# Performance work log

Hardware: AMD Instinct MI355X
Metric: run time of the kernel (lower is better)

Reference implementation:

```python
import jax, jax.numpy as jnp
import numpy as np

B, C, H_IMG, W_IMG = 16, 384, 56, 56
NUM_HEADS = 6
HEAD_DIM = C // NUM_HEADS
BN_EPS = 1e-5


def _bn(x, gamma, beta, mean, var):
    # x: [b, ch, n] or [b, ch, h, w]; per-channel affine normalization (eval-mode BatchNorm)
    shape = (1, -1) + (1,) * (x.ndim - 2)
    scale = (gamma / jnp.sqrt(var + BN_EPS)).reshape(shape)
    shift = (beta - mean * gamma / jnp.sqrt(var + BN_EPS)).reshape(shape)
    return x * scale + shift


def setup_inputs() -> dict:
    key = jax.random.key(0)
    ks = jax.random.split(key, 12)
    c2 = 2 * C
    return {
        "x": jax.random.normal(ks[0], (B, C, H_IMG, W_IMG), jnp.float32),
        "qk_w": jax.random.normal(ks[1], (c2, C // 2), jnp.float32) * 0.05,
        "qk_gamma": jax.random.uniform(ks[2], (c2,), jnp.float32, 0.5, 1.5),
        "qk_beta": jax.random.normal(ks[3], (c2,), jnp.float32) * 0.1,
        "qk_mean": jax.random.normal(ks[4], (c2,), jnp.float32) * 0.1,
        "qk_var": jax.random.uniform(ks[5], (c2,), jnp.float32, 0.5, 1.5),
        "pe_w": jax.random.normal(ks[6], (C, 1, 3, 3), jnp.float32) * 0.1,
        "pe_gamma": jax.random.uniform(ks[7], (C,), jnp.float32, 0.5, 1.5),
        "pe_beta": jax.random.normal(ks[8], (C,), jnp.float32) * 0.1,
        "pe_mean": jax.random.normal(ks[9], (C,), jnp.float32) * 0.1,
        "pe_var": jax.random.uniform(ks[10], (C,), jnp.float32, 0.5, 1.5),
    }


def reference(x, qk_w, qk_gamma, qk_beta, qk_mean, qk_var,
              pe_w, pe_gamma, pe_beta, pe_mean, pe_var):
    b, c, h, w = x.shape
    n = h * w
    s = n ** (-0.5)
    nh, hd = NUM_HEADS, HEAD_DIM

    # grouped (groups=2) 1x1 conv: out channels [0:c] from input [0:c/2], [c:2c] from [c/2:c]
    xg = x.reshape(b, 2, c // 2, n)                       # [b, 2, c/2, n]
    wg = qk_w.reshape(2, c, c // 2)                       # [group, out_per_group, in_per_group]
    qk = jnp.einsum('bgin,goi->bgon', xg, wg).reshape(b, 2 * c, n)
    qk = _bn(qk, qk_gamma, qk_beta, qk_mean, qk_var)
    qk = jax.nn.elu(qk) + 1.0

    qk = qk.reshape(b, 2, nh, hd, n)
    q, k = qk[:, 0], qk[:, 1]                             # [b, H, d, n]
    v = x.reshape(b, nh, hd, n)                           # [b, H, d, n]

    # kv = (k*s) @ (v^T * s): [b, H, d, d]
    kv = jnp.einsum('bhdn,bhen->bhde', k * s, v * s)
    # numerator: q^T @ kv -> [b, H, n, d]
    num = jnp.einsum('bhdn,bhde->bhne', q, kv)
    # denominator: q^T @ mean_n(k) -> [b, H, n]
    den = jnp.einsum('bhdn,bhd->bhn', q, k.mean(axis=-1)) + 1e-6
    attn = (num / den[..., None]).transpose(0, 1, 3, 2).reshape(b, c, h, w)

    # depthwise 3x3 conv positional encoding on v (= x) + BN
    pe = jax.lax.conv_general_dilated(
        x, pe_w, window_strides=(1, 1), padding=((1, 1), (1, 1)),
        feature_group_count=c, dimension_numbers=('NCHW', 'OIHW', 'NCHW'))
    pe = _bn(pe, pe_gamma, pe_beta, pe_mean, pe_var)

    return attn + pe
```

## Files before the change

### kernel.cpp

```cpp
#include <hip/hip_runtime.h>
#include <math.h>

#define N_SP 3136
#define BN_EPS 1e-5f

typedef __attribute__((ext_vector_type(8))) short short8;
typedef __attribute__((ext_vector_type(4))) float f32x4;

#define QK_SZ   (16*2*384*N_SP)
#define KVP_OFF (QK_SZ)
#define KVP_SZ  (16*6*7*64*80)
#define KVT_OFF (KVP_OFF + KVP_SZ)
#define KVT_FSZ (2*96*80*64/2)
#define WH_OFF  (KVT_OFF + KVT_FSZ)
#define WSPLIT_N (2*384*192)

__device__ __forceinline__ void bsplit(float f, ushort& h, ushort& l) {
    uint u = __float_as_uint(f);
    uint hr = (u + 0x7FFFu + ((u >> 16) & 1u)) >> 16;
    h = (ushort)hr;
    float fh = __uint_as_float(hr << 16);
    float fl = f - fh;
    uint v = __float_as_uint(fl);
    l = (ushort)((v + 0x7FFFu + ((v >> 16) & 1u)) >> 16);
}

__global__ __launch_bounds__(256) void p0_wsplit(
    const float* __restrict__ qk_w, ushort* __restrict__ wh, ushort* __restrict__ wl)
{
    int idx = blockIdx.x * 256 + threadIdx.x;
    if (idx >= WSPLIT_N) return;
    ushort h, l;
    bsplit(qk_w[idx], h, l);
    wh[idx] = h;
    wl[idx] = l;
}

__global__ __launch_bounds__(256) void k1_qk_mfma(
    const float* __restrict__ x, const ushort* __restrict__ wh, const ushort* __restrict__ wl,
    const float* __restrict__ gamma, const float* __restrict__ beta,
    const float* __restrict__ mean, const float* __restrict__ var,
    float* __restrict__ qk_out)
{
    __shared__ __align__(16) ushort Ah[8192];
    __shared__ __align__(16) ushort Al[8192];
    __shared__ __align__(16) ushort Bh[4096];
    __shared__ __align__(16) ushort Bl[4096];

    const int bx = blockIdx.x;
    const int by = blockIdx.y;
    const int bz = blockIdx.z;
    const int b = bz >> 1, gg = bz & 1;
    const int t = threadIdx.x;
    const int lane = t & 63, wv = t >> 6;
    const int wr = wv >> 1, wc = wv & 1;
    const int lg = lane >> 4, l15 = lane & 15;

    f32x4 acc[4][2];
    #pragma unroll
    for (int m = 0; m < 4; ++m)
        #pragma unroll
        for (int nf = 0; nf < 2; ++nf)
            acc[m][nf] = (f32x4){0.f, 0.f, 0.f, 0.f};

    const float* xg = x + (size_t)(b * 384 + gg * 192) * N_SP + bx * 64;
    const ushort* whg = wh + (gg * 384 + by * 128) * 192;
    const ushort* wlg = wl + (gg * 384 + by * 128) * 192;

    for (int kt = 0; kt < 3; ++kt) {
        #pragma unroll
        for (int li = 0; li < 4; ++li) {
            int c = li * 256 + t;
            int row = c >> 3, kb = c & 7;
            int goff = row * 192 + kt * 64 + kb * 8;
            float4 vh = *(const float4*)(whg + goff);
            float4 vl = *(const float4*)(wlg + goff);
            int ch = (row * 8 + (kb ^ (row & 7))) * 8;
            *(float4*)&Ah[ch] = vh;
            *(float4*)&Al[ch] = vl;
        }
        #pragma unroll
        for (int li = 0; li < 2; ++li) {
            int idx = li * 256 + t;
            int kp = idx >> 4;
            int nq = idx & 15;
            int k0 = kp * 2;
            const float* px = xg + (size_t)(kt * 64 + k0) * N_SP + nq * 4;
            float4 v0 = *(const float4*)px;
            float4 v1 = *(const float4*)(px + N_SP);
            ushort h0[4], l0[4], h1[4], l1[4];
            float a0[4] = {v0.x, v0.y, v0.z, v0.w};
            float a1[4] = {v1.x, v1.y, v1.z, v1.w};
            #pragma unroll
            for (int i = 0; i < 4; ++i) { bsplit(a0[i], h0[i], l0[i]); bsplit(a1[i], h1[i], l1[i]); }
            int kb = k0 >> 3, ks = (k0 & 6) >> 1;
            #pragma unroll
            for (int i = 0; i < 4; ++i) {
                int n = nq * 4 + i;
                int chunk = n * 8 + (kb ^ ((n >> 1) & 7));
                ((uint*)Bh)[chunk * 4 + ks] = (uint)h0[i] | ((uint)h1[i] << 16);
                ((uint*)Bl)[chunk * 4 + ks] = (uint)l0[i] | ((uint)l1[i] << 16);
            }
        }
        __syncthreads();
        #pragma unroll
        for (int s = 0; s < 2; ++s) {
            short8 ah[4], al[4], bh[2], bl[2];
            int kb = s * 4 + lg;
            #pragma unroll
            for (int m = 0; m < 4; ++m) {
                int row = wr * 64 + m * 16 + l15;
                int ch = (row * 8 + (kb ^ (row & 7))) * 8;
                ah[m] = *(const short8*)&Ah[ch];
                al[m] = *(const short8*)&Al[ch];
            }
            #pragma unroll
            for (int nf = 0; nf < 2; ++nf) {
                int n = wc * 32 + nf * 16 + l15;
                int ch = (n * 8 + (kb ^ ((n >> 1) & 7))) * 8;
                bh[nf] = *(const short8*)&Bh[ch];
                bl[nf] = *(const short8*)&Bl[ch];
            }
            #pragma unroll
            for (int m = 0; m < 4; ++m)
                #pragma unroll
                for (int nf = 0; nf < 2; ++nf) {
                    acc[m][nf] = __builtin_amdgcn_mfma_f32_16x16x32_bf16(ah[m], bh[nf], acc[m][nf], 0, 0, 0);
                    acc[m][nf] = __builtin_amdgcn_mfma_f32_16x16x32_bf16(ah[m], bl[nf], acc[m][nf], 0, 0, 0);
                    acc[m][nf] = __builtin_amdgcn_mfma_f32_16x16x32_bf16(al[m], bh[nf], acc[m][nf], 0, 0, 0);
                }
        }
        __syncthreads();
    }

    float* scs = (float*)Bh;
    float* shs = scs + 128;
    if (t < 128) {
        int ch = gg * 384 + by * 128 + t;
        float sc = gamma[ch] / sqrtf(var[ch] + BN_EPS);
        scs[t] = sc;
        shs[t] = beta[ch] - mean[ch] * sc;
    }
    __syncthreads();

    size_t obase = ((size_t)(b * 2 + gg) * 384 + by * 128) * N_SP + bx * 64 + wc * 32;
    #pragma unroll
    for (int m = 0; m < 4; ++m)
        #pragma unroll
        for (int nf = 0; nf < 2; ++nf) {
            #pragma unroll
            for (int r = 0; r < 4; ++r) {
                int orow = wr * 64 + m * 16 + lg * 4 + r;
                float v = acc[m][nf][r] * scs[orow] + shs[orow];
                v = v > 0.f ? v + 1.f : __expf(v);
                qk_out[obase + (size_t)orow * N_SP + nf * 16 + l15] = v;
            }
        }
}

__global__ __launch_bounds__(256) void k2_kv_mfma(
    const float* __restrict__ x, const float* __restrict__ qk,
    float* __restrict__ kv_part)
{
    __shared__ __align__(16) ushort Kh[4096], Kl[4096];
    __shared__ __align__(16) ushort Vh[5120], Vl[5120];

    const int chunk = blockIdx.x;
    const int h = blockIdx.y, b = blockIdx.z;
    const int t = threadIdx.x;
    const int lane = t & 63, wv = t >> 6;
    const int lg = lane >> 4, l15 = lane & 15;

    const float* kp = qk + (size_t)((b*2+1)*384 + h*64) * N_SP;
    const float* vp = x  + (size_t)(b*384 + h*64) * N_SP;

    #pragma unroll
    for (int li = 0; li < 4; ++li) {
        int idx = li * 256 + t;
        int row = 64 + (idx >> 6), col = idx & 63;
        int off = (row * 8 + ((col >> 3) ^ (row & 7))) * 8 + (col & 7);
        Vh[off] = (row == 64) ? (ushort)0x3F80 : (ushort)0;
        Vl[off] = 0;
    }

    f32x4 acc[5];
    #pragma unroll
    for (int nf = 0; nf < 5; ++nf) acc[nf] = (f32x4){0.f, 0.f, 0.f, 0.f};

    for (int sub = 0; sub < 7; ++sub) {
        int n0 = chunk * 448 + sub * 64;
        #pragma unroll
        for (int li = 0; li < 4; ++li) {
            int idx = li * 256 + t;
            int row = idx >> 4, sc = idx & 15;
            int off = (row * 8 + ((sc >> 1) ^ (row & 7))) * 8 + (sc & 1) * 4;
            float4 kf = *(const float4*)&kp[(size_t)row * N_SP + n0 + sc * 4];
            ushort h0,h1,h2,h3,l0,l1,l2,l3;
            bsplit(kf.x,h0,l0); bsplit(kf.y,h1,l1); bsplit(kf.z,h2,l2); bsplit(kf.w,h3,l3);
            ((uint*)&Kh[off])[0] = (uint)h0 | ((uint)h1 << 16);
            ((uint*)&Kh[off])[1] = (uint)h2 | ((uint)h3 << 16);
            ((uint*)&Kl[off])[0] = (uint)l0 | ((uint)l1 << 16);
            ((uint*)&Kl[off])[1] = (uint)l2 | ((uint)l3 << 16);
            float4 vf = *(const float4*)&vp[(size_t)row * N_SP + n0 + sc * 4];
            bsplit(vf.x,h0,l0); bsplit(vf.y,h1,l1); bsplit(vf.z,h2,l2); bsplit(vf.w,h3,l3);
            ((uint*)&Vh[off])[0] = (uint)h0 | ((uint)h1 << 16);
            ((uint*)&Vh[off])[1] = (uint)h2 | ((uint)h3 << 16);
            ((uint*)&Vl[off])[0] = (uint)l0 | ((uint)l1 << 16);
            ((uint*)&Vl[off])[1] = (uint)l2 | ((uint)l3 << 16);
        }
        __syncthreads();
        #pragma unroll
        for (int s = 0; s < 2; ++s) {
            int arow = wv * 16 + l15;
            int akb = (s * 4 + lg) ^ (arow & 7);
            short8 ah = *(const short8*)&Kh[(arow * 8 + akb) * 8];
            short8 al = *(const short8*)&Kl[(arow * 8 + akb) * 8];
            #pragma unroll
            for (int nf = 0; nf < 5; ++nf) {
                int brow = nf * 16 + l15;
                int bkb = (s * 4 + lg) ^ (brow & 7);
                short8 bh = *(const short8*)&Vh[(brow * 8 + bkb) * 8];
                short8 bl = *(const short8*)&Vl[(brow * 8 + bkb) * 8];
                acc[nf] = __builtin_amdgcn_mfma_f32_16x16x32_bf16(ah, bh, acc[nf], 0, 0, 0);
                acc[nf] = __builtin_amdgcn_mfma_f32_16x16x32_bf16(ah, bl, acc[nf], 0, 0, 0);
                acc[nf] = __builtin_amdgcn_mfma_f32_16x16x32_bf16(al, bh, acc[nf], 0, 0, 0);
            }
        }
        __syncthreads();
    }

    size_t base = (size_t)((b*6 + h)*7 + chunk) * 64 * 80;
    #pragma unroll
    for (int nf = 0; nf < 5; ++nf)
        #pragma unroll
        for (int r = 0; r < 4; ++r) {
            int d = wv * 16 + lg * 4 + r;
            kv_part[base + (size_t)d * 80 + nf * 16 + l15] = acc[nf][r];
        }
}

__global__ __launch_bounds__(256) void k2b_reduce(
    const float* __restrict__ kv_part,
    ushort* __restrict__ kvt_h, ushort* __restrict__ kvt_l)
{
    const int bh = blockIdx.x;
    const int t = threadIdx.x;
    const float inv_n = 1.0f / (float)N_SP;
    const float* base = kv_part + (size_t)bh * 7 * 64 * 80;
    ushort* oh = kvt_h + (size_t)bh * 80 * 64;
    ushort* ol = kvt_l + (size_t)bh * 80 * 64;
    for (int i = t; i < 80 * 64; i += 256) {
        int e = i >> 6, d = i & 63;
        float s = 0.f;
        if (e <= 64) {
            #pragma unroll
            for (int c = 0; c < 7; ++c) s += base[(size_t)(c * 64 + d) * 80 + e];
            s *= inv_n;
        }
        ushort h, l;
        bsplit(s, h, l);
        oh[i] = h; ol[i] = l;
    }
}

#define ATT_STRIDE 68
__global__ __launch_bounds__(256) void k3_attn_pe(
    const float* __restrict__ x, const float* __restrict__ qk,
    const ushort* __restrict__ kvt_h, const ushort* __restrict__ kvt_l,
    const float* __restrict__ pw,
    const float* __restrict__ pgamma, const float* __restrict__ pbeta,
    const float* __restrict__ pmean, const float* __restrict__ pvar,
    float* __restrict__ out)
{
    __shared__ __align__(16) float SBF[ATT_STRIDE * 64 + 64];
    ushort* Qh = (ushort*)SBF;
    ushort* Ql = Qh + 4096;

    const int bx = blockIdx.x;
    const int h = blockIdx.y, b = blockIdx.z;
    const int t = threadIdx.x;
    const int lane = t & 63, wv = t >> 6;
    const int lg = lane >> 4, l15 = lane & 15;
    const int n0 = bx * 64;
    const float* qp = qk + (size_t)((b*2+0)*384 + h*64) * N_SP + n0;

    #pragma unroll
    for (int li = 0; li < 2; ++li) {
        int idx = li * 256 + t;
        int kp2 = idx >> 4;
        int nq = idx & 15;
        int k0 = kp2 * 2;
        const float* px = qp + (size_t)k0 * N_SP + nq * 4;
        float4 v0 = *(const float4*)px;
        float4 v1 = *(const float4*)(px + N_SP);
        ushort h0[4], l0[4], h1[4], l1[4];
        float a0[4] = {v0.x, v0.y, v0.z, v0.w};
        float a1[4] = {v1.x, v1.y, v1.z, v1.w};
        #pragma unroll
        for (int i = 0; i < 4; ++i) { bsplit(a0[i], h0[i], l0[i]); bsplit(a1[i], h1[i], l1[i]); }
        int kb = k0 >> 3, ks = (k0 & 6) >> 1;
        #pragma unroll
        for (int i = 0; i < 4; ++i) {
            int n = nq * 4 + i;
            int chunk = n * 8 + (kb ^ ((n >> 1) & 7));
            ((uint*)Qh)[chunk * 4 + ks] = (uint)h0[i] | ((uint)h1[i] << 16);
            ((uint*)Ql)[chunk * 4 + ks] = (uint)l0[i] | ((uint)l1[i] << 16);
        }
    }
    __syncthreads();

    short8 bqh[2], bql[2];
    #pragma unroll
    for (int s = 0; s < 2; ++s) {
        int n = wv * 16 + l15;
        int chunk = n * 8 + ((s * 4 + lg) ^ ((n >> 1) & 7));
        bqh[s] = *(const short8*)&Qh[chunk * 8];
        bql[s] = *(const short8*)&Ql[chunk * 8];
    }
    __syncthreads();

    const ushort* ahb = kvt_h + (size_t)(b*6 + h) * 80 * 64;
    const ushort* alb = kvt_l + (size_t)(b*6 + h) * 80 * 64;
    f32x4 acc[5];
    #pragma unroll
    for (int m = 0; m < 5; ++m) acc[m] = (f32x4){0.f, 0.f, 0.f, 0.f};
    #pragma unroll
    for (int s = 0; s < 2; ++s) {
        #pragma unroll
        for (int m = 0; m < 5; ++m) {
            int off = (m * 16 + l15) * 64 + (s * 4 + lg) * 8;
            short8 ah = *(const short8*)&ahb[off];
            short8 al = *(const short8*)&alb[off];
            acc[m] = __builtin_amdgcn_mfma_f32_16x16x32_bf16(ah, bqh[s], acc[m], 0, 0, 0);
            acc[m] = __builtin_amdgcn_mfma_f32_16x16x32_bf16(ah, bql[s], acc[m], 0, 0, 0);
            acc[m] = __builtin_amdgcn_mfma_f32_16x16x32_bf16(al, bqh[s], acc[m], 0, 0, 0);
        }
    }

    {
        int ncol = wv * 16 + l15;
        #pragma unroll
        for (int m = 0; m < 4; ++m)
            #pragma unroll
            for (int r = 0; r < 4; ++r)
                SBF[(m * 16 + lg * 4 + r) * ATT_STRIDE + ncol] = acc[m][r];
        if (lg == 0)
            SBF[ATT_STRIDE * 64 + ncol] = acc[4][0];
    }
    __syncthreads();

    const int tx = t & 15, ty = t >> 4;
    const int p0 = n0 + tx * 4;
    const int y = p0 / 56, xc = p0 % 56;
    float den[4];
    #pragma unroll
    for (int p = 0; p < 4; ++p) den[p] = SBF[ATT_STRIDE * 64 + tx * 4 + p] + 1e-6f;
    #pragma unroll
    for (int j = 0; j < 4; ++j) {
        int cc = ty * 4 + j;
        int c = h * 64 + cc;
        const float* xp = x + ((size_t)b * 384 + c) * N_SP;
        float s6[3][6];
        #pragma unroll
        for (int dy = 0; dy < 3; ++dy) {
            int yy = y + dy - 1;
            bool yok = (yy >= 0) && (yy < 56);
            float4 mid = make_float4(0.f, 0.f, 0.f, 0.f);
            float lf = 0.f, rt = 0.f;
            if (yok) {
                const float* xr = xp + yy * 56;
                mid = *(const float4*)&xr[xc];
                if (xc > 0)  lf = xr[xc - 1];
                if (xc < 52) rt = xr[xc + 4];
            }
            s6[dy][0] = lf;  s6[dy][1] = mid.x; s6[dy][2] = mid.y;
            s6[dy][3] = mid.z; s6[dy][4] = mid.w; s6[dy][5] = rt;
        }
        float w9[9];
        #pragma unroll
        for (int q = 0; q < 9; ++q) w9[q] = pw[c * 9 + q];
        float sc2 = pgamma[c] / sqrtf(pvar[c] + BN_EPS);
        float sh2 = pbeta[c] - pmean[c] * sc2;
        float4 r;
        float* pr = (float*)&r;
        #pragma unroll
        for (int p = 0; p < 4; ++p) {
            float conv = 0.f;
            #pragma unroll
            for (int dy = 0; dy < 3; ++dy)
                #pragma unroll
                for (int dx = 0; dx < 3; ++dx)
                    conv += w9[dy * 3 + dx] * s6[dy][p + dx];
            float num = SBF[cc * ATT_STRIDE + tx * 4 + p];
            pr[p] = num / den[p] + (conv * sc2 + sh2);
        }
        *(float4*)&out[((size_t)b * 384 + c) * N_SP + p0] = r;
    }
}

extern "C" void kernel_launch(void* const* d_in, const int* in_sizes, int n_in,
                              void* d_out, int out_size, void* d_ws, size_t ws_size,
                              hipStream_t stream)
{
    const float* x        = (const float*)d_in[0];
    const float* qk_w     = (const float*)d_in[1];
    const float* qk_gamma = (const float*)d_in[2];
    const float* qk_beta  = (const float*)d_in[3];
    const float* qk_mean  = (const float*)d_in[4];
    const float* qk_var   = (const float*)d_in[5];
    const float* pe_w     = (const float*)d_in[6];
    const float* pe_gamma = (const float*)d_in[7];
    const float* pe_beta  = (const float*)d_in[8];
    const float* pe_mean  = (const float*)d_in[9];
    const float* pe_var   = (const float*)d_in[10];
    float* out = (float*)d_out;

    float* ws      = (float*)d_ws;
    float* qk      = ws;
    float* kv_part = ws + KVP_OFF;
    ushort* kvt_h  = (ushort*)(ws + KVT_OFF);
    ushort* kvt_l  = kvt_h + 96 * 80 * 64;
    ushort* whp    = (ushort*)(ws + WH_OFF);
    ushort* wlp    = whp + WSPLIT_N;

    hipLaunchKernelGGL(p0_wsplit, dim3((WSPLIT_N + 255)/256), dim3(256), 0, stream,
                       qk_w, whp, wlp);
    dim3 g1(49, 3, 32);
    hipLaunchKernelGGL(k1_qk_mfma, g1, dim3(256), 0, stream,
                       x, whp, wlp, qk_gamma, qk_beta, qk_mean, qk_var, qk);
    dim3 g2(7, 6, 16);
    hipLaunchKernelGGL(k2_kv_mfma, g2, dim3(256), 0, stream, x, qk, kv_part);
    hipLaunchKernelGGL(k2b_reduce, dim3(96), dim3(256), 0, stream,
                       kv_part, kvt_h, kvt_l);
    dim3 g3(49, 6, 16);
    hipLaunchKernelGGL(k3_attn_pe, g3, dim3(256), 0, stream,
                       x, qk, kvt_h, kvt_l, pe_w, pe_gamma, pe_beta, pe_mean, pe_var, out);
}
```

Measured before the change: 240.5 us.

## Store Q pre-split as bf16 hi/lo in MFMA fragment layout from the QK GEMM

The QK projection kernel now writes Q directly as bf16 hi/lo pairs packed in the per-tile layout the attention kernel's MFMA B operand expects, while K stays fp32. The attention kernel loads its Q fragments straight from global memory, with no fp32 read, split or LDS staging and two fewer barriers. The KV reduce kernel is also rewritten to read partials coalesced and transpose on write, and the QK grid axes are reordered. Q traffic drops from fp32 to two bf16 halves, but the reduce now does scattered stores and the k1 epilogue gains branching.

After: 225.4 us. -6.3%, faster.

```diff
diff --git a/kernel.cpp b/kernel.cpp
--- a/kernel.cpp
+++ b/kernel.cpp
@@ -7,8 +7,10 @@
 typedef __attribute__((ext_vector_type(8))) short short8;
 typedef __attribute__((ext_vector_type(4))) float f32x4;
 
-#define QK_SZ   (16*2*384*N_SP)
-#define KVP_OFF (QK_SZ)
+#define K_SZ    (16*384*N_SP)
+#define QF_OFF  (K_SZ)
+#define QF_FSZ  (16*6*49*8192/2)
+#define KVP_OFF (QF_OFF + QF_FSZ)
 #define KVP_SZ  (16*6*7*64*80)
 #define KVT_OFF (KVP_OFF + KVP_SZ)
 #define KVT_FSZ (2*96*80*64/2)
@@ -40,7 +42,7 @@
     const float* __restrict__ x, const ushort* __restrict__ wh, const ushort* __restrict__ wl,
     const float* __restrict__ gamma, const float* __restrict__ beta,
     const float* __restrict__ mean, const float* __restrict__ var,
-    float* __restrict__ qk_out)
+    float* __restrict__ k_out, ushort* __restrict__ qf)
 {
     __shared__ __align__(16) ushort Ah[8192];
     __shared__ __align__(16) ushort Al[8192];
@@ -48,8 +50,8 @@
     __shared__ __align__(16) ushort Bl[4096];
 
     const int bx = blockIdx.x;
-    const int by = blockIdx.y;
-    const int bz = blockIdx.z;
+    const int bz = blockIdx.y;
+    const int by = blockIdx.z;
     const int b = bz >> 1, gg = bz & 1;
     const int t = threadIdx.x;
     const int lane = t & 63, wv = t >> 6;
@@ -143,23 +145,51 @@
     }
     __syncthreads();
 
-    size_t obase = ((size_t)(b * 2 + gg) * 384 + by * 128) * N_SP + bx * 64 + wc * 32;
-    #pragma unroll
-    for (int m = 0; m < 4; ++m)
-        #pragma unroll
-        for (int nf = 0; nf < 2; ++nf) {
-            #pragma unroll
-            for (int r = 0; r < 4; ++r) {
-                int orow = wr * 64 + m * 16 + lg * 4 + r;
-                float v = acc[m][nf][r] * scs[orow] + shs[orow];
-                v = v > 0.f ? v + 1.f : __expf(v);
-                qk_out[obase + (size_t)orow * N_SP + nf * 16 + l15] = v;
-            }
-        }
+    if (gg == 0) {
+        const int head = by * 2 + wr;
+        ushort* qbase = qf + ((size_t)(b * 6 + head) * 49 + bx) * 8192;
+        #pragma unroll
+        for (int m = 0; m < 4; ++m) {
+            #pragma unroll
+            for (int nf = 0; nf < 2; ++nf) {
+                ushort hh[4], ll[4];
+                #pragma unroll
+                for (int r = 0; r < 4; ++r) {
+                    int orow = wr * 64 + m * 16 + lg * 4 + r;
+                    float v = acc[m][nf][r] * scs[orow] + shs[orow];
+                    v = v > 0.f ? v + 1.f : __expf(v);
+                    bsplit(v, hh[r], ll[r]);
+                }
+                int hc = m * 4 + lg;
+                int n = wc * 32 + nf * 16 + l15;
+                uint2 uh, ul;
+                uh.x = (uint)hh[0] | ((uint)hh[1] << 16);
+                uh.y = (uint)hh[2] | ((uint)hh[3] << 16);
+                ul.x = (uint)ll[0] | ((uint)ll[1] << 16);
+                ul.y = (uint)ll[2] | ((uint)ll[3] << 16);
+                *(uint2*)(qbase + (size_t)hc * 256 + n * 4) = uh;
+                *(uint2*)(qbase + (size_t)(16 + hc) * 256 + n * 4) = ul;
+            }
+        }
+    } else {
+        size_t obase = ((size_t)b * 384 + by * 128) * N_SP + bx * 64 + wc * 32;
+        #pragma unroll
+        for (int m = 0; m < 4; ++m)
+            #pragma unroll
+            for (int nf = 0; nf < 2; ++nf) {
+                #pragma unroll
+                for (int r = 0; r < 4; ++r) {
+                    int orow = wr * 64 + m * 16 + lg * 4 + r;
+                    float v = acc[m][nf][r] * scs[orow] + shs[orow];
+                    v = v > 0.f ? v + 1.f : __expf(v);
+                    k_out[obase + (size_t)orow * N_SP + nf * 16 + l15] = v;
+                }
+            }
+    }
 }
 
 __global__ __launch_bounds__(256) void k2_kv_mfma(
-    const float* __restrict__ x, const float* __restrict__ qk,
+    const float* __restrict__ x, const float* __restrict__ kbuf,
     float* __restrict__ kv_part)
 {
     __shared__ __align__(16) ushort Kh[4096], Kl[4096];
@@ -171,8 +201,8 @@
     const int lane = t & 63, wv = t >> 6;
     const int lg = lane >> 4, l15 = lane & 15;
 
-    const float* kp = qk + (size_t)((b*2+1)*384 + h*64) * N_SP;
-    const float* vp = x  + (size_t)(b*384 + h*64) * N_SP;
+    const float* kp = kbuf + (size_t)(b*384 + h*64) * N_SP;
+    const float* vp = x   + (size_t)(b*384 + h*64) * N_SP;
 
     #pragma unroll
     for (int li = 0; li < 4; ++li) {
@@ -246,26 +276,30 @@
     const int bh = blockIdx.x;
     const int t = threadIdx.x;
     const float inv_n = 1.0f / (float)N_SP;
-    const float* base = kv_part + (size_t)bh * 7 * 64 * 80;
-    ushort* oh = kvt_h + (size_t)bh * 80 * 64;
-    ushort* ol = kvt_l + (size_t)bh * 80 * 64;
-    for (int i = t; i < 80 * 64; i += 256) {
-        int e = i >> 6, d = i & 63;
-        float s = 0.f;
-        if (e <= 64) {
-            #pragma unroll
-            for (int c = 0; c < 7; ++c) s += base[(size_t)(c * 64 + d) * 80 + e];
-            s *= inv_n;
-        }
+    const float* base = kv_part + (size_t)bh * 7 * 5120;
+    ushort* oh = kvt_h + (size_t)bh * 5120;
+    ushort* ol = kvt_l + (size_t)bh * 5120;
+    float s[20];
+    #pragma unroll
+    for (int j = 0; j < 20; ++j) s[j] = 0.f;
+    for (int c = 0; c < 7; ++c) {
+        #pragma unroll
+        for (int j = 0; j < 20; ++j) s[j] += base[c * 5120 + j * 256 + t];
+    }
+    #pragma unroll
+    for (int j = 0; j < 20; ++j) {
+        int i = j * 256 + t;
+        int d = i / 80, e = i % 80;
         ushort h, l;
-        bsplit(s, h, l);
-        oh[i] = h; ol[i] = l;
+        bsplit(s[j] * inv_n, h, l);
+        oh[e * 64 + d] = h;
+        ol[e * 64 + d] = l;
     }
 }
 
 #define ATT_STRIDE 68
 __global__ __launch_bounds__(256) void k3_attn_pe(
-    const float* __restrict__ x, const float* __restrict__ qk,
+    const float* __restrict__ x, const ushort* __restrict__ qf,
     const ushort* __restrict__ kvt_h, const ushort* __restrict__ kvt_l,
     const float* __restrict__ pw,
     const float* __restrict__ pgamma, const float* __restrict__ pbeta,
@@ -273,8 +307,6 @@
     float* __restrict__ out)
 {
     __shared__ __align__(16) float SBF[ATT_STRIDE * 64 + 64];
-    ushort* Qh = (ushort*)SBF;
-    ushort* Ql = Qh + 4096;
 
     const int bx = blockIdx.x;
     const int h = blockIdx.y, b = blockIdx.z;
@@ -282,45 +314,26 @@
     const int lane = t & 63, wv = t >> 6;
     const int lg = lane >> 4, l15 = lane & 15;
     const int n0 = bx * 64;
-    const float* qp = qk + (size_t)((b*2+0)*384 + h*64) * N_SP + n0;
-
-    #pragma unroll
-    for (int li = 0; li < 2; ++li) {
-        int idx = li * 256 + t;
-        int kp2 = idx >> 4;
-        int nq = idx & 15;
-        int k0 = kp2 * 2;
-        const float* px = qp + (size_t)k0 * N_SP + nq * 4;
-        float4 v0 = *(const float4*)px;
-        float4 v1 = *(const float4*)(px + N_SP);
-        ushort h0[4], l0[4], h1[4], l1[4];
-        float a0[4] = {v0.x, v0.y, v0.z, v0.w};
-        float a1[4] = {v1.x, v1.y, v1.z, v1.w};
-        #pragma unroll
-        for (int i = 0; i < 4; ++i) { bsplit(a0[i], h0[i], l0[i]); bsplit(a1[i], h1[i], l1[i]); }
-        int kb = k0 >> 3, ks = (k0 & 6) >> 1;
-        #pragma unroll
-        for (int i = 0; i < 4; ++i) {
-            int n = nq * 4 + i;
-            int chunk = n * 8 + (kb ^ ((n >> 1) & 7));
-            ((uint*)Qh)[chunk * 4 + ks] = (uint)h0[i] | ((uint)h1[i] << 16);
-            ((uint*)Ql)[chunk * 4 + ks] = (uint)l0[i] | ((uint)l1[i] << 16);
-        }
-    }
-    __syncthreads();
-
+
+    const ushort* qtile = qf + ((size_t)(b * 6 + h) * 49 + bx) * 8192;
     short8 bqh[2], bql[2];
     #pragma unroll
     for (int s = 0; s < 2; ++s) {
-        int n = wv * 16 + l15;
-        int chunk = n * 8 + ((s * 4 + lg) ^ ((n >> 1) & 7));
-        bqh[s] = *(const short8*)&Qh[chunk * 8];
-        bql[s] = *(const short8*)&Ql[chunk * 8];
-    }
-    __syncthreads();
-
-    const ushort* ahb = kvt_h + (size_t)(b*6 + h) * 80 * 64;
-    const ushort* alb = kvt_l + (size_t)(b*6 + h) * 80 * 64;
+        int hc = (s * 4 + lg) * 2;
+        const ushort* ph = qtile + hc * 256 + (wv * 16 + l15) * 4;
+        uint2 a0 = *(const uint2*)ph;
+        uint2 a1 = *(const uint2*)(ph + 256);
+        uint* bh = (uint*)&bqh[s];
+        bh[0] = a0.x; bh[1] = a0.y; bh[2] = a1.x; bh[3] = a1.y;
+        const ushort* pl = ph + 16 * 256;
+        uint2 c0 = *(const uint2*)pl;
+        uint2 c1 = *(const uint2*)(pl + 256);
+        uint* blp = (uint*)&bql[s];
+        blp[0] = c0.x; blp[1] = c0.y; blp[2] = c1.x; blp[3] = c1.y;
+    }
+
+    const ushort* ahb = kvt_h + (size_t)(b * 6 + h) * 5120;
+    const ushort* alb = kvt_l + (size_t)(b * 6 + h) * 5120;
     f32x4 acc[5];
     #pragma unroll
     for (int m = 0; m < 5; ++m) acc[m] = (f32x4){0.f, 0.f, 0.f, 0.f};
@@ -416,23 +429,24 @@
     float* out = (float*)d_out;
 
     float* ws      = (float*)d_ws;
-    float* qk      = ws;
+    float* kbuf    = ws;
+    ushort* qf     = (ushort*)(ws + QF_OFF);
     float* kv_part = ws + KVP_OFF;
     ushort* kvt_h  = (ushort*)(ws + KVT_OFF);
-    ushort* kvt_l  = kvt_h + 96 * 80 * 64;
+    ushort* kvt_l  = kvt_h + 96 * 5120;
     ushort* whp    = (ushort*)(ws + WH_OFF);
     ushort* wlp    = whp + WSPLIT_N;
 
     hipLaunchKernelGGL(p0_wsplit, dim3((WSPLIT_N + 255)/256), dim3(256), 0, stream,
                        qk_w, whp, wlp);
-    dim3 g1(49, 3, 32);
+    dim3 g1(49, 32, 3);
     hipLaunchKernelGGL(k1_qk_mfma, g1, dim3(256), 0, stream,
-                       x, whp, wlp, qk_gamma, qk_beta, qk_mean, qk_var, qk);
+                       x, whp, wlp, qk_gamma, qk_beta, qk_mean, qk_var, kbuf, qf);
     dim3 g2(7, 6, 16);
-    hipLaunchKernelGGL(k2_kv_mfma, g2, dim3(256), 0, stream, x, qk, kv_part);
+    hipLaunchKernelGGL(k2_kv_mfma, g2, dim3(256), 0, stream, x, kbuf, kv_part);
     hipLaunchKernelGGL(k2b_reduce, dim3(96), dim3(256), 0, stream,
                        kv_part, kvt_h, kvt_l);
     dim3 g3(49, 6, 16);
     hipLaunchKernelGGL(k3_attn_pe, g3, dim3(256), 0, stream,
-                       x, qk, kvt_h, kvt_l, pe_w, pe_gamma, pe_beta, pe_mean, pe_var, out);
-}
+                       x, qf, kvt_h, kvt_l, pe_w, pe_gamma, pe_beta, pe_mean, pe_var, out);
+}
```
